# Optimization experiments

Measured on AMD Instinct MI355X. Metric: run time of the kernel, lower is better.

The kernel has to match this reference:

```python
import jax, jax.numpy as jnp
import numpy as np

# Model dims (see init_kwargs)
E = 512        # embedding_dim
H = 1536       # hidden_dim
SIZE = 4       # state_space.size (state types per layer)
S = 32         # choices per state type (uniform state size)
L = 12         # num_layers of child network
T = SIZE * L   # total controller steps = 48
V = SIZE * S   # num_embeddings = 128


def setup_inputs() -> dict:
    key = jax.random.key(0)
    ks = jax.random.split(key, 12)
    sc = 0.05
    f32 = jnp.float32
    return {
        "input_id": 0,
        "emb":   (jax.random.normal(ks[0], (V, E)) * sc).astype(f32),
        "W_ih1": (jax.random.normal(ks[1], (4 * H, E)) * sc).astype(f32),
        "W_hh1": (jax.random.normal(ks[2], (4 * H, H)) * sc).astype(f32),
        "b_ih1": (jax.random.normal(ks[3], (4 * H,)) * sc).astype(f32),
        "b_hh1": (jax.random.normal(ks[4], (4 * H,)) * sc).astype(f32),
        "W_ih2": (jax.random.normal(ks[5], (4 * H, H)) * sc).astype(f32),
        "W_hh2": (jax.random.normal(ks[6], (4 * H, H)) * sc).astype(f32),
        "b_ih2": (jax.random.normal(ks[7], (4 * H,)) * sc).astype(f32),
        "b_hh2": (jax.random.normal(ks[8], (4 * H,)) * sc).astype(f32),
        "W_out": (jax.random.normal(ks[9], (T, S, H)) * sc).astype(f32),
        "b_out": (jax.random.normal(ks[10], (T, S)) * sc).astype(f32),
    }


def _lstm_cell(x, h, c, Wih, Whh, bih, bhh):
    # torch.nn.LSTMCell: gates ordered (i, f, g, o)
    g = x @ Wih.T + bih + h @ Whh.T + bhh
    gi, gf, gg, go = jnp.split(g, 4)
    c_new = jax.nn.sigmoid(gf) * c + jax.nn.sigmoid(gi) * jnp.tanh(gg)
    h_new = jax.nn.sigmoid(go) * jnp.tanh(c_new)
    return h_new, c_new


def reference(input_id, emb, W_ih1, W_hh1, b_ih1, b_hh1,
              W_ih2, W_hh2, b_ih2, b_hh2, W_out, b_out):
    x0 = emb[input_id]                      # [E]
    z = jnp.zeros((H,), emb.dtype)

    def step(carry, inp):
        i, Wo, bo = inp                     # Wo: [S,H], bo: [S]
        x, h1, c1, h2, c2 = carry
        h1, c1 = _lstm_cell(x, h1, c1, W_ih1, W_hh1, b_ih1, b_hh1)
        h2, c2 = _lstm_cell(h1, h2, c2, W_ih2, W_hh2, b_ih2, b_hh2)
        logp = jax.nn.log_softmax(Wo @ h2 + bo)   # [S]
        pred = jnp.argmax(logp)
        emb_id = (i % SIZE) * S + pred            # state-space embedding id
        x_next = emb[emb_id]
        return (x_next, h1, c1, h2, c2), logp

    _, scores = jax.lax.scan(step, (x0, z, z, z, z),
                             (jnp.arange(T), W_out, b_out))
    return scores  # [T, S] log-probabilities
```

## Files before the change

### kernel.cpp

```cpp
#include <hip/hip_runtime.h>
#include <math.h>

#define H 1536
#define E 512
#define T 48
#define S 32
#define V 128
#define NB 256
#define BT 512
#define JPB 6
#define ROWS 24
#define RPW 3
#define CHK 24
#define WHH2_B   (64 * 145 * 16)
#define HBUF_B   (64 * 7 * 16)
#define DYN_LDS  (WHH2_B + HBUF_B)

__device__ __forceinline__ float sigf(float x) { return 1.0f / (1.0f + expf(-x)); }
__device__ __forceinline__ float wred(float acc) {
#pragma unroll
    for (int off = 32; off; off >>= 1) acc += __shfl_down(acc, off);
    return acc;
}

#define GLD(p)    __hip_atomic_load((p), __ATOMIC_RELAXED, __HIP_MEMORY_SCOPE_AGENT)
#define GST(p, v) __hip_atomic_store((p), (v), __ATOMIC_RELAXED, __HIP_MEMORY_SCOPE_AGENT)

__device__ __forceinline__ void gbar(unsigned* flags, unsigned& gen) {
    __syncthreads();
    gen++;
    if (threadIdx.x == 0) GST(&flags[blockIdx.x * 16], gen);
    if (threadIdx.x < 64) {
        const int i0 = threadIdx.x * 4;
        for (;;) {
            unsigned a0 = GLD(&flags[(i0 + 0) * 16]);
            unsigned a1 = GLD(&flags[(i0 + 1) * 16]);
            unsigned a2 = GLD(&flags[(i0 + 2) * 16]);
            unsigned a3 = GLD(&flags[(i0 + 3) * 16]);
            bool ok = (a0 >= gen) && (a1 >= gen) && (a2 >= gen) && (a3 >= gen);
            if (__all(ok)) break;
            __builtin_amdgcn_s_sleep(1);
        }
    }
    __syncthreads();
}

__global__ void init_kernel(unsigned* u) {
    for (int i = threadIdx.x; i < 8192; i += 256) u[i] = 0u;
}

__global__ __launch_bounds__(BT, 2) void nas_persist(
    const int* __restrict__ input_id, const float* __restrict__ emb,
    const float* __restrict__ Wih1, const float* __restrict__ Whh1,
    const float* __restrict__ bih1, const float* __restrict__ bhh1,
    const float* __restrict__ Wih2, const float* __restrict__ Whh2,
    const float* __restrict__ bih2, const float* __restrict__ bhh2,
    const float* __restrict__ Wout, const float* __restrict__ bout,
    float* __restrict__ out, float* __restrict__ ws)
{
    const int b = blockIdx.x, tid = threadIdx.x;
    const int wave = tid >> 6, lane = tid & 63;

    unsigned* flags = (unsigned*)ws + 4096;
    float* h2gp[2]  = { ws + 8192, ws + 8192 + H };
    float* candp[2] = { ws + 16384, ws + 16384 + S * H };
    float* xw1g = ws + 114688 + (size_t)b * (V * ROWS);
    float* logitp = ws + 901120;

    extern __shared__ char dyn_lds[];
    float4* whh2s = (float4*)dyn_lds;
    float*  hbuf  = (float*)(dyn_lds + WHH2_B);

    __shared__ float gacc1[ROWS], g2f[ROWS], bsum2[ROWS], zlog[S], h2f[JPB];
    __shared__ float c1s[JPB], c2s[JPB], c1cand[S * JPB];
    __shared__ int   xid_s, pred_s;

    unsigned gen = 0;

    if (tid < JPB) { c2s[tid] = 0.f; GST(h2gp[0] + b * JPB + tid, 0.f); }
    if (tid < ROWS) {
        int r = (tid / JPB) * H + b * JPB + (tid % JPB);
        bsum2[tid] = bih2[r] + bhh2[r];
    }
    if (tid == 0) xid_s = *input_id;

    {
        const int k0 = wave * RPW;
        float4 wiA[RPW], wiB[RPW];
        float  bs[RPW];
#pragma unroll
        for (int i = 0; i < RPW; ++i) {
            int k = k0 + i;
            int r = (k / JPB) * H + b * JPB + (k % JPB);
            const float4* w = (const float4*)(Wih1 + (size_t)r * E);
            wiA[i] = w[lane]; wiB[i] = w[lane + 64];
            bs[i]  = bih1[r] + bhh1[r];
        }
        float4* stage = (float4*)dyn_lds;
        for (int ch = 0; ch < 8; ++ch) {
            const float4* src = (const float4*)(emb + (size_t)ch * 16 * E);
            for (int m = tid; m < 2048; m += BT) stage[m] = src[m];
            __syncthreads();
            for (int vv = 0; vv < 16; ++vv) {
                float4 ea = stage[vv * 128 + lane];
                float4 eb = stage[vv * 128 + 64 + lane];
#pragma unroll
                for (int i = 0; i < RPW; ++i) {
                    float a = wiA[i].x * ea.x + wiA[i].y * ea.y + wiA[i].z * ea.z + wiA[i].w * ea.w
                            + wiB[i].x * eb.x + wiB[i].y * eb.y + wiB[i].z * eb.z + wiB[i].w * eb.w;
                    a = wred(a);
                    if (lane == 0) xw1g[(ch * 16 + vv) * ROWS + (k0 + i)] = a + bs[i];
                }
            }
            __syncthreads();
        }
    }

    for (int k = 0; k < ROWS; ++k) {
        int r = (k / JPB) * H + b * JPB + (k % JPB);
        const float4* src = (const float4*)(Whh2 + (size_t)r * H);
        if (tid < 384) {
            int l = tid / 6, j = tid % 6;
            whh2s[l * 145 + k * 6 + j] = src[tid];
        }
    }
    __syncthreads();

    float w1[RPW][CHK], w2[RPW][CHK];
#pragma unroll
    for (int i = 0; i < RPW; ++i) {
        int k = wave * RPW + i;
        int r = (k / JPB) * H + b * JPB + (k % JPB);
        const float4* p1 = (const float4*)(Whh1 + (size_t)r * H) + lane * 6;
        const float4* p2 = (const float4*)(Wih2 + (size_t)r * H) + lane * 6;
#pragma unroll
        for (int j = 0; j < 6; ++j) {
            float4 v1 = p1[j], v2 = p2[j];
            w1[i][4 * j + 0] = v1.x; w1[i][4 * j + 1] = v1.y;
            w1[i][4 * j + 2] = v1.z; w1[i][4 * j + 3] = v1.w;
            w2[i][4 * j + 0] = v2.x; w2[i][4 * j + 1] = v2.y;
            w2[i][4 * j + 2] = v2.z; w2[i][4 * j + 3] = v2.w;
        }
    }
    __syncthreads();

    if (tid < JPB) {
        const float* xr = xw1g + (size_t)xid_s * ROWS;
        float gi = xr[tid], gg = xr[2 * JPB + tid], go = xr[3 * JPB + tid];
        float cn = sigf(gi) * tanhf(gg);
        c1s[tid] = cn;
        GST(candp[0] + b * JPB + tid, sigf(go) * tanhf(cn));
    }
    gbar(flags, gen);

    const int m0 = (tid / CHK) * 28 + (tid % CHK);
    const int m1 = ((tid + 512) / CHK) * 28 + ((tid + 512) % CHK);
    const int m2 = ((tid + 1024) / CHK) * 28 + ((tid + 1024) % CHK);

    for (int k = 0; k <= T; ++k) {
        float wcol[JPB];
        if (k < T && wave == 0 && lane < S) {
            const float* wp = Wout + ((size_t)k * S + lane) * H + b * JPB;
#pragma unroll
            for (int j = 0; j < JPB; ++j) wcol[j] = wp[j];
        }
        const float* h2src = h2gp[k & 1];
        float u0 = GLD(h2src + tid);
        float u1 = GLD(h2src + tid + 512);
        float u2 = GLD(h2src + tid + 1024);

        if (k > 0) {
            const float* lp = logitp + (size_t)(k & 1) * (S * NB)
                              + (tid >> 4) * NB + (tid & 15) * 16;
            float acc = 0.f;
#pragma unroll
            for (int i = 0; i < 16; ++i) acc += GLD(lp + i);
#pragma unroll
            for (int off = 8; off; off >>= 1) acc += __shfl_down(acc, off, 16);
            if ((tid & 15) == 0)
                zlog[tid >> 4] = acc + bout[(size_t)(k - 1) * S + (tid >> 4)];
        }
        __syncthreads();
        if (k > 0) {
            if (wave == 0) {
                float z = (lane < S) ? zlog[lane] : -1e30f;
                float v = z; int idx = (lane < S) ? lane : 9999;
#pragma unroll
                for (int off = 32; off; off >>= 1) {
                    float ov = __shfl_xor(v, off); int oi = __shfl_xor(idx, off);
                    if (ov > v || (ov == v && oi < idx)) { v = ov; idx = oi; }
                }
                float e = (lane < S) ? expf(z - v) : 0.f;
#pragma unroll
                for (int off = 32; off; off >>= 1) e += __shfl_xor(e, off);
                if (lane == 0) pred_s = idx;
                if (b == 0 && lane < S) out[(size_t)(k - 1) * S + lane] = z - v - logf(e);
            }
            __syncthreads();
        }
        if (k == T) return;
        const int psel = (k > 0) ? pred_s : 0;
        if (k > 0 && tid < JPB) c1s[tid] = c1cand[psel * JPB + tid];

        const float* h1src = candp[k & 1] + (size_t)psel * H;
        float t0 = GLD(h1src + tid);
        float t1 = GLD(h1src + tid + 512);
        float t2 = GLD(h1src + tid + 1024);

        hbuf[m0] = u0; hbuf[m1] = u1; hbuf[m2] = u2;
        __syncthreads();
        float h2c[CHK];
        {
            const float4* hp = (const float4*)hbuf + lane * 7;
#pragma unroll
            for (int j = 0; j < 6; ++j) {
                float4 v = hp[j];
                h2c[4 * j + 0] = v.x; h2c[4 * j + 1] = v.y;
                h2c[4 * j + 2] = v.z; h2c[4 * j + 3] = v.w;
            }
        }
        float ahv[RPW];
#pragma unroll
        for (int i = 0; i < RPW; ++i) {
            int kk = wave * RPW + i;
            const float4* wp = whh2s + lane * 145 + kk * 6;
            float ah = 0.f;
#pragma unroll
            for (int j = 0; j < 6; ++j) {
                float4 v = wp[j];
                ah += v.x * h2c[4 * j + 0] + v.y * h2c[4 * j + 1]
                    + v.z * h2c[4 * j + 2] + v.w * h2c[4 * j + 3];
            }
            ahv[i] = wred(ah);
        }
        __syncthreads();
        hbuf[m0] = t0; hbuf[m1] = t1; hbuf[m2] = t2;
        __syncthreads();
        float h1c[CHK];
        {
            const float4* hp = (const float4*)hbuf + lane * 7;
#pragma unroll
            for (int j = 0; j < 6; ++j) {
                float4 v = hp[j];
                h1c[4 * j + 0] = v.x; h1c[4 * j + 1] = v.y;
                h1c[4 * j + 2] = v.z; h1c[4 * j + 3] = v.w;
            }
        }
        float a1[RPW], a2[RPW];
#pragma unroll
        for (int i = 0; i < RPW; ++i) { a1[i] = 0.f; a2[i] = 0.f; }
#pragma unroll
        for (int kk = 0; kk < CHK; ++kk) {
            float h = h1c[kk];
#pragma unroll
            for (int i = 0; i < RPW; ++i) {
                a1[i] += w1[i][kk] * h;
                a2[i] += w2[i][kk] * h;
            }
        }
#pragma unroll
        for (int i = 0; i < RPW; ++i) {
            int kk = wave * RPW + i;
            float s1 = wred(a1[i]);
            float s2 = wred(a2[i]);
            if (lane == 0) {
                gacc1[kk] = s1;
                g2f[kk]   = s2 + ahv[i] + bsum2[kk];
            }
        }
        __syncthreads();

        if (tid < JPB) {
            float gi = g2f[tid],           gf = g2f[JPB + tid];
            float gg = g2f[2 * JPB + tid], go = g2f[3 * JPB + tid];
            float cn = sigf(gf) * c2s[tid] + sigf(gi) * tanhf(gg);
            c2s[tid] = cn;
            float hn = sigf(go) * tanhf(cn);
            h2f[tid] = hn;
            GST(h2gp[(k + 1) & 1] + b * JPB + tid, hn);
        }
        if (tid < S * JPB) {
            int p = tid / JPB, j = tid % JPB;
            const float* xr = xw1g + (size_t)((k & 3) * S + p) * ROWS;
            float gi = gacc1[j]           + xr[j];
            float gf = gacc1[JPB + j]     + xr[JPB + j];
            float gg = gacc1[2 * JPB + j] + xr[2 * JPB + j];
            float go = gacc1[3 * JPB + j] + xr[3 * JPB + j];
            float cn = sigf(gf) * c1s[j] + sigf(gi) * tanhf(gg);
            c1cand[tid] = cn;
            GST(candp[(k + 1) & 1] + (size_t)p * H + b * JPB + j,
                sigf(go) * tanhf(cn));
        }
        __syncthreads();
        if (wave == 0 && lane < S) {
            float p = 0.f;
#pragma unroll
            for (int j = 0; j < JPB; ++j) p += wcol[j] * h2f[j];
            GST(logitp + (size_t)((k + 1) & 1) * (S * NB) + lane * NB + b, p);
        }
        gbar(flags, gen);
    }
}

extern "C" void kernel_launch(void* const* d_in, const int* in_sizes, int n_in,
                              void* d_out, int out_size, void* d_ws, size_t ws_size,
                              hipStream_t stream) {
    const int*   input_id = (const int*)d_in[0];
    const float* emb  = (const float*)d_in[1];
    const float* Wih1 = (const float*)d_in[2];
    const float* Whh1 = (const float*)d_in[3];
    const float* bih1 = (const float*)d_in[4];
    const float* bhh1 = (const float*)d_in[5];
    const float* Wih2 = (const float*)d_in[6];
    const float* Whh2 = (const float*)d_in[7];
    const float* bih2 = (const float*)d_in[8];
    const float* bhh2 = (const float*)d_in[9];
    const float* Wout = (const float*)d_in[10];
    const float* bout = (const float*)d_in[11];
    float* out = (float*)d_out;
    float* ws  = (float*)d_ws;

    init_kernel<<<1, 256, 0, stream>>>((unsigned*)ws);

    void* args[] = { (void*)&input_id, (void*)&emb,
                     (void*)&Wih1, (void*)&Whh1, (void*)&bih1, (void*)&bhh1,
                     (void*)&Wih2, (void*)&Whh2, (void*)&bih2, (void*)&bhh2,
                     (void*)&Wout, (void*)&bout, (void*)&out, (void*)&ws };
    hipLaunchCooperativeKernel((void*)nas_persist, dim3(NB), dim3(BT), args,
                               DYN_LDS, stream);
}
```

Baseline: 1.147 ms.

## Replace grid barrier with generation-tagged data flags for point-to-point sync

Removes the per-step global barrier and instead packs each published value (h2, candidate h1, partial logits) with a generation tag in a 64-bit word, so consumers spin only until the specific data they need is ready. This lets blocks proceed as soon as their inputs arrive instead of waiting for all 256 blocks, and overlaps the h2 load with the logit reduction. It doubles the bytes of the exchanged data, makes the init kernel zero a much larger workspace, and relaxes launch bounds to one block per CU.

```diff
diff --git a/kernel.cpp b/kernel.cpp
--- a/kernel.cpp
+++ b/kernel.cpp
@@ -16,6 +16,14 @@
 #define HBUF_B   (64 * 7 * 16)
 #define DYN_LDS  (WHH2_B + HBUF_B)
 
+typedef unsigned long long u64;
+
+#define H2_U64    4096
+#define CAND_U64  8192
+#define LOG_U64   106496
+#define ZERO_W    245760
+#define XW1_W     245760
+
 __device__ __forceinline__ float sigf(float x) { return 1.0f / (1.0f + expf(-x)); }
 __device__ __forceinline__ float wred(float acc) {
 #pragma unroll
@@ -23,33 +31,22 @@
     return acc;
 }
 
-#define GLD(p)    __hip_atomic_load((p), __ATOMIC_RELAXED, __HIP_MEMORY_SCOPE_AGENT)
-#define GST(p, v) __hip_atomic_store((p), (v), __ATOMIC_RELAXED, __HIP_MEMORY_SCOPE_AGENT)
-
-__device__ __forceinline__ void gbar(unsigned* flags, unsigned& gen) {
-    __syncthreads();
-    gen++;
-    if (threadIdx.x == 0) GST(&flags[blockIdx.x * 16], gen);
-    if (threadIdx.x < 64) {
-        const int i0 = threadIdx.x * 4;
-        for (;;) {
-            unsigned a0 = GLD(&flags[(i0 + 0) * 16]);
-            unsigned a1 = GLD(&flags[(i0 + 1) * 16]);
-            unsigned a2 = GLD(&flags[(i0 + 2) * 16]);
-            unsigned a3 = GLD(&flags[(i0 + 3) * 16]);
-            bool ok = (a0 >= gen) && (a1 >= gen) && (a2 >= gen) && (a3 >= gen);
-            if (__all(ok)) break;
-            __builtin_amdgcn_s_sleep(1);
-        }
-    }
-    __syncthreads();
-}
+#define GLD64(p)    __hip_atomic_load((p), __ATOMIC_RELAXED, __HIP_MEMORY_SCOPE_AGENT)
+#define GST64(p, v) __hip_atomic_store((p), (v), __ATOMIC_RELAXED, __HIP_MEMORY_SCOPE_AGENT)
+
+__device__ __forceinline__ u64 pk(float v, unsigned g) {
+    return ((u64)g << 32) | (u64)__float_as_uint(v);
+}
+__device__ __forceinline__ float    pvf(u64 x) { return __uint_as_float((unsigned)x); }
+__device__ __forceinline__ unsigned ptg(u64 x) { return (unsigned)(x >> 32); }
 
 __global__ void init_kernel(unsigned* u) {
-    for (int i = threadIdx.x; i < 8192; i += 256) u[i] = 0u;
-}
-
-__global__ __launch_bounds__(BT, 2) void nas_persist(
+    for (int i = blockIdx.x * blockDim.x + threadIdx.x; i < ZERO_W;
+         i += gridDim.x * blockDim.x)
+        u[i] = 0u;
+}
+
+__global__ __launch_bounds__(BT, 1) void nas_persist(
     const int* __restrict__ input_id, const float* __restrict__ emb,
     const float* __restrict__ Wih1, const float* __restrict__ Whh1,
     const float* __restrict__ bih1, const float* __restrict__ bhh1,
@@ -61,11 +58,10 @@
     const int b = blockIdx.x, tid = threadIdx.x;
     const int wave = tid >> 6, lane = tid & 63;
 
-    unsigned* flags = (unsigned*)ws + 4096;
-    float* h2gp[2]  = { ws + 8192, ws + 8192 + H };
-    float* candp[2] = { ws + 16384, ws + 16384 + S * H };
-    float* xw1g = ws + 114688 + (size_t)b * (V * ROWS);
-    float* logitp = ws + 901120;
+    u64* h2t    = (u64*)ws + H2_U64;
+    u64* candt  = (u64*)ws + CAND_U64;
+    u64* logitt = (u64*)ws + LOG_U64;
+    float* xw1g = ws + XW1_W + (size_t)b * (V * ROWS);
 
     extern __shared__ char dyn_lds[];
     float4* whh2s = (float4*)dyn_lds;
@@ -75,9 +71,10 @@
     __shared__ float c1s[JPB], c2s[JPB], c1cand[S * JPB];
     __shared__ int   xid_s, pred_s;
 
-    unsigned gen = 0;
-
-    if (tid < JPB) { c2s[tid] = 0.f; GST(h2gp[0] + b * JPB + tid, 0.f); }
+    if (tid < JPB) {
+        c2s[tid] = 0.f;
+        GST64(h2t + b * JPB + tid, pk(0.f, 1u));
+    }
     if (tid < ROWS) {
         int r = (tid / JPB) * H + b * JPB + (tid % JPB);
         bsum2[tid] = bih2[r] + bhh2[r];
@@ -149,38 +146,66 @@
         float gi = xr[tid], gg = xr[2 * JPB + tid], go = xr[3 * JPB + tid];
         float cn = sigf(gi) * tanhf(gg);
         c1s[tid] = cn;
-        GST(candp[0] + b * JPB + tid, sigf(go) * tanhf(cn));
-    }
-    gbar(flags, gen);
+        GST64(candt + b * JPB + tid, pk(sigf(go) * tanhf(cn), 1u));
+    }
 
     const int m0 = (tid / CHK) * 28 + (tid % CHK);
     const int m1 = ((tid + 512) / CHK) * 28 + ((tid + 512) % CHK);
     const int m2 = ((tid + 1024) / CHK) * 28 + ((tid + 1024) % CHK);
 
     for (int k = 0; k <= T; ++k) {
+        const unsigned expg = (unsigned)(k + 1);
+
+        const u64* h2src = h2t + (size_t)(k & 1) * H;
+        u64 hv0 = 0, hv1 = 0, hv2 = 0;
+        if (k < T) {
+            hv0 = GLD64(h2src + tid);
+            hv1 = GLD64(h2src + tid + 512);
+            hv2 = GLD64(h2src + tid + 1024);
+        }
+
+        if (k > 0) {
+            const u64* lp = logitt + (size_t)(k & 1) * (S * NB)
+                            + (tid >> 4) * NB + (tid & 15) * 16;
+            u64 pvv[16];
+            for (;;) {
+                bool ok = true;
+#pragma unroll
+                for (int i = 0; i < 16; ++i) pvv[i] = GLD64(lp + i);
+#pragma unroll
+                for (int i = 0; i < 16; ++i) ok &= (ptg(pvv[i]) >= expg);
+                if (ok) break;
+                __builtin_amdgcn_s_sleep(1);
+            }
+            float acc = 0.f;
+#pragma unroll
+            for (int i = 0; i < 16; ++i) acc += pvf(pvv[i]);
+#pragma unroll
+            for (int off = 8; off; off >>= 1) acc += __shfl_down(acc, off, 16);
+            if ((tid & 15) == 0)
+                zlog[tid >> 4] = acc + bout[(size_t)(k - 1) * S + (tid >> 4)];
+        }
+
         float wcol[JPB];
         if (k < T && wave == 0 && lane < S) {
             const float* wp = Wout + ((size_t)k * S + lane) * H + b * JPB;
 #pragma unroll
             for (int j = 0; j < JPB; ++j) wcol[j] = wp[j];
         }
-        const float* h2src = h2gp[k & 1];
-        float u0 = GLD(h2src + tid);
-        float u1 = GLD(h2src + tid + 512);
-        float u2 = GLD(h2src + tid + 1024);
-
-        if (k > 0) {
-            const float* lp = logitp + (size_t)(k & 1) * (S * NB)
-                              + (tid >> 4) * NB + (tid & 15) * 16;
-            float acc = 0.f;
-#pragma unroll
-            for (int i = 0; i < 16; ++i) acc += GLD(lp + i);
-#pragma unroll
-            for (int off = 8; off; off >>= 1) acc += __shfl_down(acc, off, 16);
-            if ((tid & 15) == 0)
-                zlog[tid >> 4] = acc + bout[(size_t)(k - 1) * S + (tid >> 4)];
-        }
-        __syncthreads();
+
+        if (k < T) {
+            for (;;) {
+                bool ok = (ptg(hv0) >= expg) && (ptg(hv1) >= expg) && (ptg(hv2) >= expg);
+                if (ok) break;
+                __builtin_amdgcn_s_sleep(1);
+                hv0 = GLD64(h2src + tid);
+                hv1 = GLD64(h2src + tid + 512);
+                hv2 = GLD64(h2src + tid + 1024);
+            }
+            hbuf[m0] = pvf(hv0); hbuf[m1] = pvf(hv1); hbuf[m2] = pvf(hv2);
+        }
+        __syncthreads();
+
         if (k > 0) {
             if (wave == 0) {
                 float z = (lane < S) ? zlog[lane] : -1e30f;
@@ -202,13 +227,11 @@
         const int psel = (k > 0) ? pred_s : 0;
         if (k > 0 && tid < JPB) c1s[tid] = c1cand[psel * JPB + tid];
 
-        const float* h1src = candp[k & 1] + (size_t)psel * H;
-        float t0 = GLD(h1src + tid);
-        float t1 = GLD(h1src + tid + 512);
-        float t2 = GLD(h1src + tid + 1024);
-
-        hbuf[m0] = u0; hbuf[m1] = u1; hbuf[m2] = u2;
-        __syncthreads();
+        const u64* h1src = candt + (size_t)(k & 1) * (S * H) + (size_t)psel * H;
+        u64 tv0 = GLD64(h1src + tid);
+        u64 tv1 = GLD64(h1src + tid + 512);
+        u64 tv2 = GLD64(h1src + tid + 1024);
+
         float h2c[CHK];
         {
             const float4* hp = (const float4*)hbuf + lane * 7;
@@ -234,8 +257,18 @@
             ahv[i] = wred(ah);
         }
         __syncthreads();
-        hbuf[m0] = t0; hbuf[m1] = t1; hbuf[m2] = t2;
-        __syncthreads();
+
+        for (;;) {
+            bool ok = (ptg(tv0) >= expg) && (ptg(tv1) >= expg) && (ptg(tv2) >= expg);
+            if (ok) break;
+            __builtin_amdgcn_s_sleep(1);
+            tv0 = GLD64(h1src + tid);
+            tv1 = GLD64(h1src + tid + 512);
+            tv2 = GLD64(h1src + tid + 1024);
+        }
+        hbuf[m0] = pvf(tv0); hbuf[m1] = pvf(tv1); hbuf[m2] = pvf(tv2);
+        __syncthreads();
+
         float h1c[CHK];
         {
             const float4* hp = (const float4*)hbuf + lane * 7;
@@ -270,6 +303,7 @@
         }
         __syncthreads();
 
+        const unsigned newg = (unsigned)(k + 2);
         if (tid < JPB) {
             float gi = g2f[tid],           gf = g2f[JPB + tid];
             float gg = g2f[2 * JPB + tid], go = g2f[3 * JPB + tid];
@@ -277,7 +311,7 @@
             c2s[tid] = cn;
             float hn = sigf(go) * tanhf(cn);
             h2f[tid] = hn;
-            GST(h2gp[(k + 1) & 1] + b * JPB + tid, hn);
+            GST64(h2t + (size_t)((k + 1) & 1) * H + b * JPB + tid, pk(hn, newg));
         }
         if (tid < S * JPB) {
             int p = tid / JPB, j = tid % JPB;
@@ -288,17 +322,17 @@
             float go = gacc1[3 * JPB + j] + xr[3 * JPB + j];
             float cn = sigf(gf) * c1s[j] + sigf(gi) * tanhf(gg);
             c1cand[tid] = cn;
-            GST(candp[(k + 1) & 1] + (size_t)p * H + b * JPB + j,
-                sigf(go) * tanhf(cn));
+            GST64(candt + (size_t)((k + 1) & 1) * (S * H) + (size_t)p * H + b * JPB + j,
+                  pk(sigf(go) * tanhf(cn), newg));
         }
         __syncthreads();
         if (wave == 0 && lane < S) {
             float p = 0.f;
 #pragma unroll
             for (int j = 0; j < JPB; ++j) p += wcol[j] * h2f[j];
-            GST(logitp + (size_t)((k + 1) & 1) * (S * NB) + lane * NB + b, p);
-        }
-        gbar(flags, gen);
+            GST64(logitt + (size_t)((k + 1) & 1) * (S * NB) + lane * NB + b,
+                  pk(p, newg));
+        }
     }
 }
 
@@ -320,7 +354,7 @@
     float* out = (float*)d_out;
     float* ws  = (float*)d_ws;
 
-    init_kernel<<<1, 256, 0, stream>>>((unsigned*)ws);
+    init_kernel<<<256, 256, 0, stream>>>((unsigned*)ws);
 
     void* args[] = { (void*)&input_id, (void*)&emb,
                      (void*)&Wih1, (void*)&Whh1, (void*)&bih1, (void*)&bhh1,
```

Result: slower. 1.431 ms (+24.7%).

## Replace grid barrier with generation-tagged logit and prediction handoff

Applied to the files above, without the earlier changes.

Removes the all-to-all flag barrier at each step. Every block now writes its partial logits as a 64-bit value carrying a generation tag. Block 0 spins until all tagged partials for the step have arrived, then computes the softmax and argmax and publishes the predicted index, also tagged. The other blocks wait only on that single prediction word, which cuts polling traffic and the extra barrier round. The trade-offs are that ordering of the h2 and candidate buffers now relies on relaxed atomics ordered only through the logit chain, block 0 sits on the critical path, and launch bounds drop to one block per SIMD group.

```diff
diff --git a/kernel.cpp b/kernel.cpp
--- a/kernel.cpp
+++ b/kernel.cpp
@@ -16,6 +16,15 @@
 #define HBUF_B   (64 * 7 * 16)
 #define DYN_LDS  (WHH2_B + HBUF_B)
 
+typedef unsigned long long u64;
+
+#define PRED_U64  0
+#define LOG_U64   2048
+#define H2_W      36864
+#define CAND_W    40960
+#define XW1_W     139264
+#define ZERO_W    36864
+
 __device__ __forceinline__ float sigf(float x) { return 1.0f / (1.0f + expf(-x)); }
 __device__ __forceinline__ float wred(float acc) {
 #pragma unroll
@@ -23,33 +32,27 @@
     return acc;
 }
 
-#define GLD(p)    __hip_atomic_load((p), __ATOMIC_RELAXED, __HIP_MEMORY_SCOPE_AGENT)
-#define GST(p, v) __hip_atomic_store((p), (v), __ATOMIC_RELAXED, __HIP_MEMORY_SCOPE_AGENT)
-
-__device__ __forceinline__ void gbar(unsigned* flags, unsigned& gen) {
-    __syncthreads();
-    gen++;
-    if (threadIdx.x == 0) GST(&flags[blockIdx.x * 16], gen);
-    if (threadIdx.x < 64) {
-        const int i0 = threadIdx.x * 4;
-        for (;;) {
-            unsigned a0 = GLD(&flags[(i0 + 0) * 16]);
-            unsigned a1 = GLD(&flags[(i0 + 1) * 16]);
-            unsigned a2 = GLD(&flags[(i0 + 2) * 16]);
-            unsigned a3 = GLD(&flags[(i0 + 3) * 16]);
-            bool ok = (a0 >= gen) && (a1 >= gen) && (a2 >= gen) && (a3 >= gen);
-            if (__all(ok)) break;
-            __builtin_amdgcn_s_sleep(1);
-        }
-    }
-    __syncthreads();
-}
+#define GLD(p)      __hip_atomic_load((p), __ATOMIC_RELAXED, __HIP_MEMORY_SCOPE_AGENT)
+#define GST(p, v)   __hip_atomic_store((p), (v), __ATOMIC_RELAXED, __HIP_MEMORY_SCOPE_AGENT)
+#define GLD64(p)    __hip_atomic_load((p), __ATOMIC_RELAXED, __HIP_MEMORY_SCOPE_AGENT)
+#define GST64(p, v) __hip_atomic_store((p), (v), __ATOMIC_RELAXED, __HIP_MEMORY_SCOPE_AGENT)
+
+__device__ __forceinline__ u64 pkf(float v, unsigned g) {
+    return ((u64)g << 32) | (u64)__float_as_uint(v);
+}
+__device__ __forceinline__ u64 pki(int v, unsigned g) {
+    return ((u64)g << 32) | (u64)(unsigned)v;
+}
+__device__ __forceinline__ float    pvf(u64 x) { return __uint_as_float((unsigned)x); }
+__device__ __forceinline__ unsigned ptg(u64 x) { return (unsigned)(x >> 32); }
 
 __global__ void init_kernel(unsigned* u) {
-    for (int i = threadIdx.x; i < 8192; i += 256) u[i] = 0u;
-}
-
-__global__ __launch_bounds__(BT, 2) void nas_persist(
+    for (int i = blockIdx.x * blockDim.x + threadIdx.x; i < ZERO_W;
+         i += gridDim.x * blockDim.x)
+        u[i] = 0u;
+}
+
+__global__ __launch_bounds__(BT, 1) void nas_persist(
     const int* __restrict__ input_id, const float* __restrict__ emb,
     const float* __restrict__ Wih1, const float* __restrict__ Whh1,
     const float* __restrict__ bih1, const float* __restrict__ bhh1,
@@ -61,11 +64,11 @@
     const int b = blockIdx.x, tid = threadIdx.x;
     const int wave = tid >> 6, lane = tid & 63;
 
-    unsigned* flags = (unsigned*)ws + 4096;
-    float* h2gp[2]  = { ws + 8192, ws + 8192 + H };
-    float* candp[2] = { ws + 16384, ws + 16384 + S * H };
-    float* xw1g = ws + 114688 + (size_t)b * (V * ROWS);
-    float* logitp = ws + 901120;
+    u64* predt  = (u64*)ws + PRED_U64;
+    u64* logitt = (u64*)ws + LOG_U64;
+    float* h2gp[2]  = { ws + H2_W,   ws + H2_W + H };
+    float* candp[2] = { ws + CAND_W, ws + CAND_W + S * H };
+    float* xw1g = ws + XW1_W + (size_t)b * (V * ROWS);
 
     extern __shared__ char dyn_lds[];
     float4* whh2s = (float4*)dyn_lds;
@@ -74,8 +77,6 @@
     __shared__ float gacc1[ROWS], g2f[ROWS], bsum2[ROWS], zlog[S], h2f[JPB];
     __shared__ float c1s[JPB], c2s[JPB], c1cand[S * JPB];
     __shared__ int   xid_s, pred_s;
-
-    unsigned gen = 0;
 
     if (tid < JPB) { c2s[tid] = 0.f; GST(h2gp[0] + b * JPB + tid, 0.f); }
     if (tid < ROWS) {
@@ -151,7 +152,8 @@
         c1s[tid] = cn;
         GST(candp[0] + b * JPB + tid, sigf(go) * tanhf(cn));
     }
-    gbar(flags, gen);
+    __syncthreads();
+    if (tid == 0) GST64(logitt + b, pkf(0.f, 1u));
 
     const int m0 = (tid / CHK) * 28 + (tid % CHK);
     const int m1 = ((tid + 512) / CHK) * 28 + ((tid + 512) % CHK);
@@ -164,44 +166,85 @@
 #pragma unroll
             for (int j = 0; j < JPB; ++j) wcol[j] = wp[j];
         }
+
+        if (b == 0) {
+            if (k == 0) {
+                if (tid < 64) {
+                    const u64* lp = logitt + tid * 4;
+                    for (;;) {
+                        bool ok = (ptg(GLD64(lp + 0)) >= 1u) && (ptg(GLD64(lp + 1)) >= 1u)
+                               && (ptg(GLD64(lp + 2)) >= 1u) && (ptg(GLD64(lp + 3)) >= 1u);
+                        if (__all(ok)) break;
+                        __builtin_amdgcn_s_sleep(1);
+                    }
+                }
+                __syncthreads();
+                if (tid == 0) { pred_s = 0; GST64(predt, pki(0, 1u)); }
+                __syncthreads();
+            } else {
+                const unsigned eg = (unsigned)(k + 1);
+                const u64* lp = logitt + (size_t)(k & 1) * (S * NB)
+                                + (tid >> 4) * NB + (tid & 15) * 16;
+                u64 pvv[16];
+                for (;;) {
+                    bool ok = true;
+#pragma unroll
+                    for (int i = 0; i < 16; ++i) pvv[i] = GLD64(lp + i);
+#pragma unroll
+                    for (int i = 0; i < 16; ++i) ok &= (ptg(pvv[i]) >= eg);
+                    if (ok) break;
+                    __builtin_amdgcn_s_sleep(1);
+                }
+                float acc = 0.f;
+#pragma unroll
+                for (int i = 0; i < 16; ++i) acc += pvf(pvv[i]);
+#pragma unroll
+                for (int off = 8; off; off >>= 1) acc += __shfl_down(acc, off, 16);
+                if ((tid & 15) == 0)
+                    zlog[tid >> 4] = acc + bout[(size_t)(k - 1) * S + (tid >> 4)];
+                __syncthreads();
+                if (wave == 0) {
+                    float z = (lane < S) ? zlog[lane] : -1e30f;
+                    float v = z; int idx = (lane < S) ? lane : 9999;
+#pragma unroll
+                    for (int off = 32; off; off >>= 1) {
+                        float ov = __shfl_xor(v, off); int oi = __shfl_xor(idx, off);
+                        if (ov > v || (ov == v && oi < idx)) { v = ov; idx = oi; }
+                    }
+                    float e = (lane < S) ? expf(z - v) : 0.f;
+#pragma unroll
+                    for (int off = 32; off; off >>= 1) e += __shfl_xor(e, off);
+                    if (lane == 0) {
+                        pred_s = idx;
+                        GST64(predt, pki(idx, (unsigned)(k + 1)));
+                    }
+                    if (lane < S) out[(size_t)(k - 1) * S + lane] = z - v - logf(e);
+                }
+                __syncthreads();
+            }
+        } else {
+            if (k == T) return;
+            if (tid == 0) {
+                const unsigned eg = (unsigned)(k + 1);
+                u64 v;
+                for (;;) {
+                    v = GLD64(predt);
+                    if (ptg(v) >= eg) break;
+                    __builtin_amdgcn_s_sleep(1);
+                }
+                pred_s = (int)(unsigned)v;
+            }
+            __syncthreads();
+        }
+        if (k == T) return;
+
+        const int psel = pred_s;
+        if (k > 0 && tid < JPB) c1s[tid] = c1cand[psel * JPB + tid];
+
         const float* h2src = h2gp[k & 1];
         float u0 = GLD(h2src + tid);
         float u1 = GLD(h2src + tid + 512);
         float u2 = GLD(h2src + tid + 1024);
-
-        if (k > 0) {
-            const float* lp = logitp + (size_t)(k & 1) * (S * NB)
-                              + (tid >> 4) * NB + (tid & 15) * 16;
-            float acc = 0.f;
-#pragma unroll
-            for (int i = 0; i < 16; ++i) acc += GLD(lp + i);
-#pragma unroll
-            for (int off = 8; off; off >>= 1) acc += __shfl_down(acc, off, 16);
-            if ((tid & 15) == 0)
-                zlog[tid >> 4] = acc + bout[(size_t)(k - 1) * S + (tid >> 4)];
-        }
-        __syncthreads();
-        if (k > 0) {
-            if (wave == 0) {
-                float z = (lane < S) ? zlog[lane] : -1e30f;
-                float v = z; int idx = (lane < S) ? lane : 9999;
-#pragma unroll
-                for (int off = 32; off; off >>= 1) {
-                    float ov = __shfl_xor(v, off); int oi = __shfl_xor(idx, off);
-                    if (ov > v || (ov == v && oi < idx)) { v = ov; idx = oi; }
-                }
-                float e = (lane < S) ? expf(z - v) : 0.f;
-#pragma unroll
-                for (int off = 32; off; off >>= 1) e += __shfl_xor(e, off);
-                if (lane == 0) pred_s = idx;
-                if (b == 0 && lane < S) out[(size_t)(k - 1) * S + lane] = z - v - logf(e);
-            }
-            __syncthreads();
-        }
-        if (k == T) return;
-        const int psel = (k > 0) ? pred_s : 0;
-        if (k > 0 && tid < JPB) c1s[tid] = c1cand[psel * JPB + tid];
-
         const float* h1src = candp[k & 1] + (size_t)psel * H;
         float t0 = GLD(h1src + tid);
         float t1 = GLD(h1src + tid + 512);
@@ -296,9 +339,9 @@
             float p = 0.f;
 #pragma unroll
             for (int j = 0; j < JPB; ++j) p += wcol[j] * h2f[j];
-            GST(logitp + (size_t)((k + 1) & 1) * (S * NB) + lane * NB + b, p);
-        }
-        gbar(flags, gen);
+            GST64(logitt + (size_t)((k + 1) & 1) * (S * NB) + lane * NB + b,
+                  pkf(p, (unsigned)(k + 2)));
+        }
     }
 }
 
@@ -320,7 +363,7 @@
     float* out = (float*)d_out;
     float* ws  = (float*)d_ws;
 
-    init_kernel<<<1, 256, 0, stream>>>((unsigned*)ws);
+    init_kernel<<<64, 256, 0, stream>>>((unsigned*)ws);
 
     void* args[] = { (void*)&input_id, (void*)&emb,
                      (void*)&Wih1, (void*)&Whh1, (void*)&bih1, (void*)&bhh1,
```

After: 1.186 ms. 3.3% more time.

## Replace grid barrier with generation-tagged h2 values and redundant per-block logits

Applied to the files above, without the earlier changes.

Drops the flag-based global barrier and instead stores each h2 element as a 64-bit word holding the value and a generation tag. Consumers spin on the tags of exactly the data they need. Each block now recomputes the full 32-logit output projection from the gathered h2, so the cross-block partial-logit reduction buffer and its extra global round trip go away. The cost is redundant Wout reads in every block (about 196 KB per step per block) and a launch bound lowered to one block per SM. The candidate h1 buffer is still double-buffered with no explicit barrier; correctness relies on the h2 tag ordering implying the candp writes are visible, and relaxed atomics may not guarantee that.

```diff
diff --git a/kernel.cpp b/kernel.cpp
--- a/kernel.cpp
+++ b/kernel.cpp
@@ -16,6 +16,11 @@
 #define HBUF_B   (64 * 7 * 16)
 #define DYN_LDS  (WHH2_B + HBUF_B)
 
+typedef unsigned long long u64;
+
+#define CAND_W  8192
+#define XW1_W   106496
+
 __device__ __forceinline__ float sigf(float x) { return 1.0f / (1.0f + expf(-x)); }
 __device__ __forceinline__ float wred(float acc) {
 #pragma unroll
@@ -23,33 +28,18 @@
     return acc;
 }
 
-#define GLD(p)    __hip_atomic_load((p), __ATOMIC_RELAXED, __HIP_MEMORY_SCOPE_AGENT)
-#define GST(p, v) __hip_atomic_store((p), (v), __ATOMIC_RELAXED, __HIP_MEMORY_SCOPE_AGENT)
-
-__device__ __forceinline__ void gbar(unsigned* flags, unsigned& gen) {
-    __syncthreads();
-    gen++;
-    if (threadIdx.x == 0) GST(&flags[blockIdx.x * 16], gen);
-    if (threadIdx.x < 64) {
-        const int i0 = threadIdx.x * 4;
-        for (;;) {
-            unsigned a0 = GLD(&flags[(i0 + 0) * 16]);
-            unsigned a1 = GLD(&flags[(i0 + 1) * 16]);
-            unsigned a2 = GLD(&flags[(i0 + 2) * 16]);
-            unsigned a3 = GLD(&flags[(i0 + 3) * 16]);
-            bool ok = (a0 >= gen) && (a1 >= gen) && (a2 >= gen) && (a3 >= gen);
-            if (__all(ok)) break;
-            __builtin_amdgcn_s_sleep(1);
-        }
-    }
-    __syncthreads();
+#define GLD(p)      __hip_atomic_load((p), __ATOMIC_RELAXED, __HIP_MEMORY_SCOPE_AGENT)
+#define GST(p, v)   __hip_atomic_store((p), (v), __ATOMIC_RELAXED, __HIP_MEMORY_SCOPE_AGENT)
+#define GLD64(p)    __hip_atomic_load((p), __ATOMIC_RELAXED, __HIP_MEMORY_SCOPE_AGENT)
+#define GST64(p, v) __hip_atomic_store((p), (v), __ATOMIC_RELAXED, __HIP_MEMORY_SCOPE_AGENT)
+
+__device__ __forceinline__ u64 pkf(float v, unsigned g) {
+    return ((u64)g << 32) | (u64)__float_as_uint(v);
 }
-
-__global__ void init_kernel(unsigned* u) {
-    for (int i = threadIdx.x; i < 8192; i += 256) u[i] = 0u;
-}
-
-__global__ __launch_bounds__(BT, 2) void nas_persist(
+__device__ __forceinline__ float    pvf(u64 x) { return __uint_as_float((unsigned)x); }
+__device__ __forceinline__ unsigned ptg(u64 x) { return (unsigned)(x >> 32); }
+
+__global__ __launch_bounds__(BT, 1) void nas_persist(
     const int* __restrict__ input_id, const float* __restrict__ emb,
     const float* __restrict__ Wih1, const float* __restrict__ Whh1,
     const float* __restrict__ bih1, const float* __restrict__ bhh1,
@@ -61,23 +51,19 @@
     const int b = blockIdx.x, tid = threadIdx.x;
     const int wave = tid >> 6, lane = tid & 63;
 
-    unsigned* flags = (unsigned*)ws + 4096;
-    float* h2gp[2]  = { ws + 8192, ws + 8192 + H };
-    float* candp[2] = { ws + 16384, ws + 16384 + S * H };
-    float* xw1g = ws + 114688 + (size_t)b * (V * ROWS);
-    float* logitp = ws + 901120;
+    u64* h2t = (u64*)ws;
+    float* candp[2] = { ws + CAND_W, ws + CAND_W + S * H };
+    float* xw1g = ws + XW1_W + (size_t)b * (V * ROWS);
 
     extern __shared__ char dyn_lds[];
     float4* whh2s = (float4*)dyn_lds;
     float*  hbuf  = (float*)(dyn_lds + WHH2_B);
 
-    __shared__ float gacc1[ROWS], g2f[ROWS], bsum2[ROWS], zlog[S], h2f[JPB];
+    __shared__ float gacc1[ROWS], g2f[ROWS], bsum2[ROWS], zlog[S];
     __shared__ float c1s[JPB], c2s[JPB], c1cand[S * JPB];
     __shared__ int   xid_s, pred_s;
 
-    unsigned gen = 0;
-
-    if (tid < JPB) { c2s[tid] = 0.f; GST(h2gp[0] + b * JPB + tid, 0.f); }
+    if (tid < JPB) c2s[tid] = 0.f;
     if (tid < ROWS) {
         int r = (tid / JPB) * H + b * JPB + (tid % JPB);
         bsum2[tid] = bih2[r] + bhh2[r];
@@ -151,54 +137,104 @@
         c1s[tid] = cn;
         GST(candp[0] + b * JPB + tid, sigf(go) * tanhf(cn));
     }
-    gbar(flags, gen);
+    __syncthreads();
+    if (tid < JPB)
+        GST64(h2t + b * JPB + tid, pkf(0.f, 1u));
 
     const int m0 = (tid / CHK) * 28 + (tid % CHK);
     const int m1 = ((tid + 512) / CHK) * 28 + ((tid + 512) % CHK);
     const int m2 = ((tid + 1024) / CHK) * 28 + ((tid + 1024) % CHK);
 
     for (int k = 0; k <= T; ++k) {
-        float wcol[JPB];
-        if (k < T && wave == 0 && lane < S) {
-            const float* wp = Wout + ((size_t)k * S + lane) * H + b * JPB;
-#pragma unroll
-            for (int j = 0; j < JPB; ++j) wcol[j] = wp[j];
-        }
-        const float* h2src = h2gp[k & 1];
-        float u0 = GLD(h2src + tid);
-        float u1 = GLD(h2src + tid + 512);
-        float u2 = GLD(h2src + tid + 1024);
-
-        if (k > 0) {
-            const float* lp = logitp + (size_t)(k & 1) * (S * NB)
-                              + (tid >> 4) * NB + (tid & 15) * 16;
-            float acc = 0.f;
-#pragma unroll
-            for (int i = 0; i < 16; ++i) acc += GLD(lp + i);
-#pragma unroll
-            for (int off = 8; off; off >>= 1) acc += __shfl_down(acc, off, 16);
-            if ((tid & 15) == 0)
-                zlog[tid >> 4] = acc + bout[(size_t)(k - 1) * S + (tid >> 4)];
-        }
-        __syncthreads();
-        if (k > 0) {
-            if (wave == 0) {
-                float z = (lane < S) ? zlog[lane] : -1e30f;
-                float v = z; int idx = (lane < S) ? lane : 9999;
-#pragma unroll
-                for (int off = 32; off; off >>= 1) {
-                    float ov = __shfl_xor(v, off); int oi = __shfl_xor(idx, off);
-                    if (ov > v || (ov == v && oi < idx)) { v = ov; idx = oi; }
+        if (k == T && b != 0) return;
+
+        float4 wo[4][6];
+        if (k >= 1) {
+#pragma unroll
+            for (int q = 0; q < 4; ++q) {
+                const float4* wp = (const float4*)(Wout
+                    + ((size_t)(k - 1) * S + (wave * 4 + q)) * H) + lane * 6;
+#pragma unroll
+                for (int j = 0; j < 6; ++j) wo[q][j] = wp[j];
+            }
+        }
+
+        const unsigned expg = (unsigned)(k + 1);
+        const u64* h2src = h2t + (size_t)(k & 1) * H;
+        u64 a0 = GLD64(h2src + tid);
+        u64 a1 = GLD64(h2src + tid + 512);
+        u64 a2 = GLD64(h2src + tid + 1024);
+        for (;;) {
+            if ((ptg(a0) >= expg) && (ptg(a1) >= expg) && (ptg(a2) >= expg)) break;
+            __builtin_amdgcn_s_sleep(1);
+            a0 = GLD64(h2src + tid);
+            a1 = GLD64(h2src + tid + 512);
+            a2 = GLD64(h2src + tid + 1024);
+        }
+        hbuf[m0] = pvf(a0); hbuf[m1] = pvf(a1); hbuf[m2] = pvf(a2);
+        __syncthreads();
+
+        float h2c[CHK];
+        {
+            const float4* hp = (const float4*)hbuf + lane * 7;
+#pragma unroll
+            for (int j = 0; j < 6; ++j) {
+                float4 v = hp[j];
+                h2c[4 * j + 0] = v.x; h2c[4 * j + 1] = v.y;
+                h2c[4 * j + 2] = v.z; h2c[4 * j + 3] = v.w;
+            }
+        }
+
+        if (k >= 1) {
+#pragma unroll
+            for (int q = 0; q < 4; ++q) {
+                float acc = 0.f;
+#pragma unroll
+                for (int j = 0; j < 6; ++j) {
+                    float4 v = wo[q][j];
+                    acc += v.x * h2c[4 * j + 0] + v.y * h2c[4 * j + 1]
+                         + v.z * h2c[4 * j + 2] + v.w * h2c[4 * j + 3];
                 }
-                float e = (lane < S) ? expf(z - v) : 0.f;
-#pragma unroll
-                for (int off = 32; off; off >>= 1) e += __shfl_xor(e, off);
-                if (lane == 0) pred_s = idx;
-                if (b == 0 && lane < S) out[(size_t)(k - 1) * S + lane] = z - v - logf(e);
-            }
-            __syncthreads();
-        }
+                acc = wred(acc);
+                if (lane == 0)
+                    zlog[wave * 4 + q] = acc + bout[(size_t)(k - 1) * S + (wave * 4 + q)];
+            }
+        }
+        __syncthreads();
+
+        if (k >= 1 && wave == 0) {
+            float z = (lane < S) ? zlog[lane] : -1e30f;
+            float v = z; int idx = (lane < S) ? lane : 9999;
+#pragma unroll
+            for (int off = 32; off; off >>= 1) {
+                float ov = __shfl_xor(v, off); int oi = __shfl_xor(idx, off);
+                if (ov > v || (ov == v && oi < idx)) { v = ov; idx = oi; }
+            }
+            float e = (lane < S) ? expf(z - v) : 0.f;
+#pragma unroll
+            for (int off = 32; off; off >>= 1) e += __shfl_xor(e, off);
+            if (lane == 0) pred_s = idx;
+            if (b == 0 && lane < S) out[(size_t)(k - 1) * S + lane] = z - v - logf(e);
+        }
+        float ahv[RPW];
+        if (k < T) {
+#pragma unroll
+            for (int i = 0; i < RPW; ++i) {
+                int kk = wave * RPW + i;
+                const float4* wp = whh2s + lane * 145 + kk * 6;
+                float ah = 0.f;
+#pragma unroll
+                for (int j = 0; j < 6; ++j) {
+                    float4 v = wp[j];
+                    ah += v.x * h2c[4 * j + 0] + v.y * h2c[4 * j + 1]
+                        + v.z * h2c[4 * j + 2] + v.w * h2c[4 * j + 3];
+                }
+                ahv[i] = wred(ah);
+            }
+        }
+        __syncthreads();
         if (k == T) return;
+
         const int psel = (k > 0) ? pred_s : 0;
         if (k > 0 && tid < JPB) c1s[tid] = c1cand[psel * JPB + tid];
 
@@ -206,36 +242,9 @@
         float t0 = GLD(h1src + tid);
         float t1 = GLD(h1src + tid + 512);
         float t2 = GLD(h1src + tid + 1024);
-
-        hbuf[m0] = u0; hbuf[m1] = u1; hbuf[m2] = u2;
-        __syncthreads();
-        float h2c[CHK];
-        {
-            const float4* hp = (const float4*)hbuf + lane * 7;
-#pragma unroll
-            for (int j = 0; j < 6; ++j) {
-                float4 v = hp[j];
-                h2c[4 * j + 0] = v.x; h2c[4 * j + 1] = v.y;
-                h2c[4 * j + 2] = v.z; h2c[4 * j + 3] = v.w;
-            }
-        }
-        float ahv[RPW];
-#pragma unroll
-        for (int i = 0; i < RPW; ++i) {
-            int kk = wave * RPW + i;
-            const float4* wp = whh2s + lane * 145 + kk * 6;
-            float ah = 0.f;
-#pragma unroll
-            for (int j = 0; j < 6; ++j) {
-                float4 v = wp[j];
-                ah += v.x * h2c[4 * j + 0] + v.y * h2c[4 * j + 1]
-                    + v.z * h2c[4 * j + 2] + v.w * h2c[4 * j + 3];
-            }
-            ahv[i] = wred(ah);
-        }
-        __syncthreads();
         hbuf[m0] = t0; hbuf[m1] = t1; hbuf[m2] = t2;
         __syncthreads();
+
         float h1c[CHK];
         {
             const float4* hp = (const float4*)hbuf + lane * 7;
@@ -246,23 +255,23 @@
                 h1c[4 * j + 2] = v.z; h1c[4 * j + 3] = v.w;
             }
         }
-        float a1[RPW], a2[RPW];
-#pragma unroll
-        for (int i = 0; i < RPW; ++i) { a1[i] = 0.f; a2[i] = 0.f; }
+        float a1v[RPW], a2v[RPW];
+#pragma unroll
+        for (int i = 0; i < RPW; ++i) { a1v[i] = 0.f; a2v[i] = 0.f; }
 #pragma unroll
         for (int kk = 0; kk < CHK; ++kk) {
             float h = h1c[kk];
 #pragma unroll
             for (int i = 0; i < RPW; ++i) {
-                a1[i] += w1[i][kk] * h;
-                a2[i] += w2[i][kk] * h;
+                a1v[i] += w1[i][kk] * h;
+                a2v[i] += w2[i][kk] * h;
             }
         }
 #pragma unroll
         for (int i = 0; i < RPW; ++i) {
             int kk = wave * RPW + i;
-            float s1 = wred(a1[i]);
-            float s2 = wred(a2[i]);
+            float s1 = wred(a1v[i]);
+            float s2 = wred(a2v[i]);
             if (lane == 0) {
                 gacc1[kk] = s1;
                 g2f[kk]   = s2 + ahv[i] + bsum2[kk];
@@ -270,14 +279,13 @@
         }
         __syncthreads();
 
+        float hn = 0.f;
         if (tid < JPB) {
             float gi = g2f[tid],           gf = g2f[JPB + tid];
             float gg = g2f[2 * JPB + tid], go = g2f[3 * JPB + tid];
             float cn = sigf(gf) * c2s[tid] + sigf(gi) * tanhf(gg);
             c2s[tid] = cn;
-            float hn = sigf(go) * tanhf(cn);
-            h2f[tid] = hn;
-            GST(h2gp[(k + 1) & 1] + b * JPB + tid, hn);
+            hn = sigf(go) * tanhf(cn);
         }
         if (tid < S * JPB) {
             int p = tid / JPB, j = tid % JPB;
@@ -292,13 +300,9 @@
                 sigf(go) * tanhf(cn));
         }
         __syncthreads();
-        if (wave == 0 && lane < S) {
-            float p = 0.f;
-#pragma unroll
-            for (int j = 0; j < JPB; ++j) p += wcol[j] * h2f[j];
-            GST(logitp + (size_t)((k + 1) & 1) * (S * NB) + lane * NB + b, p);
-        }
-        gbar(flags, gen);
+        if (tid < JPB)
+            GST64(h2t + (size_t)((k + 1) & 1) * H + b * JPB + tid,
+                  pkf(hn, (unsigned)(k + 2)));
     }
 }
 
@@ -320,7 +324,7 @@
     float* out = (float*)d_out;
     float* ws  = (float*)d_ws;
 
-    init_kernel<<<1, 256, 0, stream>>>((unsigned*)ws);
+    hipMemsetAsync(d_ws, 0, 2 * H * sizeof(u64), stream);
 
     void* args[] = { (void*)&input_id, (void*)&emb,
                      (void*)&Wih1, (void*)&Whh1, (void*)&bih1, (void*)&bhh1,
```

New measurement: 1.355 ms. 18.1% more time.
